# Kernel optimization log

Hardware: AMD Instinct MI355X
Metric: run time of the kernel (lower is better)

## Reference

```python
import jax, jax.numpy as jnp
import numpy as np

N = 100000   # nodes
E = 1200000  # edges
D = 64       # feature dim (in_channels == out_channels)


def gcn_layer(x, W, src, dst):
    # GCNConv(normalize=False, bias=False, aggr='add'):
    # linear transform then scatter-add of source messages into targets.
    h = x @ W                                            # [N, D]
    msg = h[src]                                         # [E, D] gather
    return jax.ops.segment_sum(msg, dst, num_segments=x.shape[0])  # [N, D]


def setup_inputs() -> dict:
    key = jax.random.key(0)
    ks = jax.random.split(key, 5)
    x = jax.random.normal(ks[0], (N, D), dtype=jnp.float32)
    edge_index = jax.random.randint(ks[1], (2, E), 0, N, dtype=jnp.int64)
    scale = 1.0 / np.sqrt(D).astype(np.float32)
    W0 = jax.random.normal(ks[2], (D, D), dtype=jnp.float32) * scale
    W1 = jax.random.normal(ks[3], (D, D), dtype=jnp.float32) * scale
    W2 = jax.random.normal(ks[4], (D, D), dtype=jnp.float32) * scale
    return {"x": x, "edge_index": edge_index, "W0": W0, "W1": W1, "W2": W2}


def reference(x, edge_index, W0, W1, W2):
    src = edge_index[0]  # messages flow source -> target (PyG default)
    dst = edge_index[1]
    # num_hop = 3 stacked convs; dropout p=0 and use_bn=False are no-ops.
    for W in (W0, W1, W2):
        x = gcn_layer(x, W, src, dst)
    return x
```

## Files before the change

kernel.cpp:

```cpp
#include <hip/hip_runtime.h>


#define GCN_D 64
#define SEGSHIFT 8
#define SEGROWS 256
#define MAXSEG 512
#define A_EPB 4096
#define HISTB 512

typedef unsigned short ushort;

__device__ __forceinline__ float bf2f(ushort u) {
    union { unsigned u; float f; } c; c.u = ((unsigned)u) << 16; return c.f;
}
__device__ __forceinline__ float bflo(unsigned u) {
    union { unsigned u; float f; } c; c.u = u << 16; return c.f;
}
__device__ __forceinline__ float bfhi(unsigned u) {
    union { unsigned u; float f; } c; c.u = u & 0xFFFF0000u; return c.f;
}
__device__ __forceinline__ ushort f2bf(float f) {
    union { float f; unsigned u; } c; c.f = f;
    const unsigned r = 0x7FFFu + ((c.u >> 16) & 1u);
    return (ushort)((c.u + r) >> 16);
}
__device__ __forceinline__ unsigned pack2(float a, float b) {
    return (unsigned)f2bf(a) | ((unsigned)f2bf(b) << 16);
}

__global__ __launch_bounds__(256) void k_wchain(const float* __restrict__ W0,
                                                const float* __restrict__ W1,
                                                const float* __restrict__ W2,
                                                float* __restrict__ Wc,
                                                int* __restrict__ ghist,
                                                int* __restrict__ csr0) {
    __shared__ float A[4096], B[4096], T[4096];
    const int t = threadIdx.x;
    for (int i = t; i < MAXSEG; i += 256) { ghist[i] = 0; csr0[i] = 0; }
    for (int i = t; i < 1024; i += 256) {
        ((float4*)A)[i] = ((const float4*)W0)[i];
        ((float4*)B)[i] = ((const float4*)W1)[i];
    }
    __syncthreads();
#pragma unroll
    for (int g = 0; g < 4; ++g) {
        const int idx = t + 256 * g;
        const int r = idx >> 4, c4 = idx & 15;
        float4 acc = make_float4(0.f, 0.f, 0.f, 0.f);
#pragma unroll
        for (int k = 0; k < 64; ++k) {
            const float a = A[r * 64 + k];
            const float4 b = ((float4*)B)[k * 16 + c4];
            acc.x = fmaf(a, b.x, acc.x); acc.y = fmaf(a, b.y, acc.y);
            acc.z = fmaf(a, b.z, acc.z); acc.w = fmaf(a, b.w, acc.w);
        }
        ((float4*)T)[idx] = acc;
    }
    __syncthreads();
    for (int i = t; i < 1024; i += 256) ((float4*)B)[i] = ((const float4*)W2)[i];
    __syncthreads();
#pragma unroll
    for (int g = 0; g < 4; ++g) {
        const int idx = t + 256 * g;
        const int r = idx >> 4, c4 = idx & 15;
        float4 acc = make_float4(0.f, 0.f, 0.f, 0.f);
#pragma unroll
        for (int k = 0; k < 64; ++k) {
            const float a = T[r * 64 + k];
            const float4 b = ((float4*)B)[k * 16 + c4];
            acc.x = fmaf(a, b.x, acc.x); acc.y = fmaf(a, b.y, acc.y);
            acc.z = fmaf(a, b.z, acc.z); acc.w = fmaf(a, b.w, acc.w);
        }
        ((float4*)Wc)[idx] = acc;
    }
}

__global__ __launch_bounds__(256, 3) void k_gemmcvt(const float* __restrict__ X,
                                                    const float* __restrict__ Wc,
                                                    ushort* __restrict__ B,
                                                    const int* __restrict__ ei,
                                                    int* __restrict__ ghist,
                                                    int nrows, int E) {
    __shared__ float Wl[4096];
    __shared__ float Xl[64][68];
    __shared__ int h[MAXSEG];
    const int tid = threadIdx.x;
    for (int i = tid; i < 1024; i += 256) ((float4*)Wl)[i] = ((const float4*)Wc)[i];

    const int rowBase = blockIdx.x * 64;
    for (int i = tid; i < 1024; i += 256) {
        const int r = i >> 4, c4 = i & 15;
        const int gr = rowBase + r;
        const float4 v = (gr < nrows) ? ((const float4*)X)[(size_t)gr * 16 + c4]
                                      : make_float4(0.f, 0.f, 0.f, 0.f);
        *(float4*)&Xl[r][c4 * 4] = v;
    }
    __syncthreads();

    const int tr = tid >> 4;
    const int tc = tid & 15;
    float4 a0 = make_float4(0.f, 0.f, 0.f, 0.f);
    float4 a1 = a0, a2 = a0, a3 = a0;
#pragma unroll 8
    for (int k = 0; k < 64; ++k) {
        const float4 w4 = ((const float4*)Wl)[k * 16 + tc];
        const float x0 = Xl[tr][k];
        const float x1 = Xl[tr + 16][k];
        const float x2 = Xl[tr + 32][k];
        const float x3 = Xl[tr + 48][k];
        a0.x = fmaf(x0, w4.x, a0.x); a0.y = fmaf(x0, w4.y, a0.y);
        a0.z = fmaf(x0, w4.z, a0.z); a0.w = fmaf(x0, w4.w, a0.w);
        a1.x = fmaf(x1, w4.x, a1.x); a1.y = fmaf(x1, w4.y, a1.y);
        a1.z = fmaf(x1, w4.z, a1.z); a1.w = fmaf(x1, w4.w, a1.w);
        a2.x = fmaf(x2, w4.x, a2.x); a2.y = fmaf(x2, w4.y, a2.y);
        a2.z = fmaf(x2, w4.z, a2.z); a2.w = fmaf(x2, w4.w, a2.w);
        a3.x = fmaf(x3, w4.x, a3.x); a3.y = fmaf(x3, w4.y, a3.y);
        a3.z = fmaf(x3, w4.z, a3.z); a3.w = fmaf(x3, w4.w, a3.w);
    }
    {
        const int r0 = rowBase + tr;
        ushort4 o;
        if (r0 < nrows) {
            o.x = f2bf(a0.x); o.y = f2bf(a0.y); o.z = f2bf(a0.z); o.w = f2bf(a0.w);
            ((ushort4*)B)[(size_t)r0 * 16 + tc] = o;
        }
        if (r0 + 16 < nrows) {
            o.x = f2bf(a1.x); o.y = f2bf(a1.y); o.z = f2bf(a1.z); o.w = f2bf(a1.w);
            ((ushort4*)B)[(size_t)(r0 + 16) * 16 + tc] = o;
        }
        if (r0 + 32 < nrows) {
            o.x = f2bf(a2.x); o.y = f2bf(a2.y); o.z = f2bf(a2.z); o.w = f2bf(a2.w);
            ((ushort4*)B)[(size_t)(r0 + 32) * 16 + tc] = o;
        }
        if (r0 + 48 < nrows) {
            o.x = f2bf(a3.x); o.y = f2bf(a3.y); o.z = f2bf(a3.z); o.w = f2bf(a3.w);
            ((ushort4*)B)[(size_t)(r0 + 48) * 16 + tc] = o;
        }
    }

    if (blockIdx.x < HISTB) {
        for (int i = tid; i < MAXSEG; i += 256) h[i] = 0;
        __syncthreads();
        for (int e = blockIdx.x * 256 + tid; e < E; e += HISTB * 256)
            atomicAdd(&h[ei[E + e] >> SEGSHIFT], 1);
        __syncthreads();
        for (int i = tid; i < MAXSEG; i += 256) {
            const int c = h[i];
            if (c) atomicAdd(&ghist[i], c);
        }
    }
}

__global__ __launch_bounds__(512) void k_apart(const int* __restrict__ ei,
                                               const int* __restrict__ ghist,
                                               int* __restrict__ csr0,
                                               unsigned* __restrict__ ebuf, int E) {
    __shared__ int hist[MAXSEG], lofs[MAXSEG], cur[MAXSEG], gbase[MAXSEG], goffx[MAXSEG];
    __shared__ unsigned stg[A_EPB];
    __shared__ ushort stg2[A_EPB];
    const int t = threadIdx.x;
    const int base = blockIdx.x * A_EPB;
    const int cnt = min(A_EPB, E - base);

    const int gv = ghist[t];
    goffx[t] = gv; __syncthreads();
    for (int off = 1; off < MAXSEG; off <<= 1) {
        const int y = (t >= off) ? goffx[t - off] : 0;
        __syncthreads();
        goffx[t] += y;
        __syncthreads();
    }
    const int gexcl = goffx[t] - gv;
    goffx[t] = gexcl;
    hist[t] = 0;
    __syncthreads();

    unsigned my[8]; int mb[8];
#pragma unroll
    for (int j = 0; j < 8; ++j) {
        const int i = t + j * 512;
        if (i < cnt) {
            const int e = base + i;
            const unsigned s = (unsigned)ei[e];
            const unsigned d = (unsigned)ei[E + e];
            my[j] = (s << 8) | (d & (SEGROWS - 1));
            mb[j] = (int)(d >> SEGSHIFT);
            atomicAdd(&hist[mb[j]], 1);
        } else mb[j] = -1;
    }
    __syncthreads();

    {
        const int v = hist[t];
        lofs[t] = v; __syncthreads();
        for (int off = 1; off < MAXSEG; off <<= 1) {
            const int y = (t >= off) ? lofs[t - off] : 0;
            __syncthreads();
            lofs[t] += y;
            __syncthreads();
        }
        const int excl = lofs[t] - v;
        __syncthreads();
        lofs[t] = excl; cur[t] = excl;
    }
    __syncthreads();

#pragma unroll
    for (int j = 0; j < 8; ++j) {
        if (mb[j] >= 0) {
            const int p = atomicAdd(&cur[mb[j]], 1);
            stg[p] = my[j];
            stg2[p] = (ushort)mb[j];
        }
    }
    __syncthreads();

    {
        const int c = hist[t];
        const int p = c ? atomicAdd(&csr0[t], c) : 0;
        gbase[t] = goffx[t] + p;
    }
    __syncthreads();

    for (int i = t; i < cnt; i += 512) {
        const int b = (int)stg2[i];
        ebuf[(size_t)gbase[b] + (unsigned)(i - lofs[b])] = stg[i];
    }
}

__global__ __launch_bounds__(SEGROWS) void k_bplace(const unsigned* __restrict__ ebuf,
                                                    const int* __restrict__ ghist,
                                                    int* __restrict__ rp,
                                                    int* __restrict__ cs, int N, int E) {
    __shared__ int h[SEGROWS], ofs[SEGROWS], gpart[SEGROWS];
    __shared__ int gx[MAXSEG];
    const int s = blockIdx.x;
    const int t = threadIdx.x;

    const int a0 = ghist[2 * t];
    const int a1 = ghist[2 * t + 1];
    const int ps = a0 + a1;
    gpart[t] = ps; __syncthreads();
    for (int off = 1; off < SEGROWS; off <<= 1) {
        const int y = (t >= off) ? gpart[t - off] : 0;
        __syncthreads();
        gpart[t] += y;
        __syncthreads();
    }
    const int ex = gpart[t] - ps;
    gx[2 * t] = ex;
    gx[2 * t + 1] = ex + a0;
    if (s == 0 && t == 0) rp[N] = E;
    __syncthreads();

    const int e0 = gx[s];
    const int e1 = e0 + ghist[s];

    h[t] = 0; __syncthreads();
    for (int e = e0 + t; e < e1; e += SEGROWS)
        atomicAdd(&h[ebuf[e] & (SEGROWS - 1)], 1);
    __syncthreads();

    const int v = h[t];
    ofs[t] = v; __syncthreads();
    for (int off = 1; off < SEGROWS; off <<= 1) {
        const int y = (t >= off) ? ofs[t - off] : 0;
        __syncthreads();
        ofs[t] += y;
        __syncthreads();
    }
    const int excl = ofs[t] - v;
    const int r = s * SEGROWS + t;
    if (r < N) rp[r] = e0 + excl;
    __syncthreads();
    ofs[t] = excl;
    __syncthreads();

    for (int e = e0 + t; e < e1; e += SEGROWS) {
        const unsigned pr = ebuf[e];
        const int lr = (int)(pr & (SEGROWS - 1));
        const int p = atomicAdd(&ofs[lr], 1);
        cs[e0 + p] = (int)(pr >> 8);
    }
}

__global__ __launch_bounds__(256) void k_aggc2(const ushort* __restrict__ B,
                                               const int* __restrict__ rp,
                                               const int* __restrict__ cs,
                                               ushort* __restrict__ out, int N) {
    const int t = threadIdx.x;
    const int gw = (blockIdx.x * 256 + t) >> 6;
    const int lane = t & 63;
    const int f8 = lane & 7;
    const int r = gw * 8 + (lane >> 3);
    if (r >= N) return;

    const int e0 = rp[r];
    const int e1 = rp[r + 1];
    const uint4* Bv = (const uint4*)B;

    float acc[8] = {0.f, 0.f, 0.f, 0.f, 0.f, 0.f, 0.f, 0.f};
    int e = e0;
    for (; e + 7 < e1; e += 8) {
        uint4 u[8];
#pragma unroll
        for (int j = 0; j < 8; ++j) u[j] = Bv[(size_t)cs[e + j] * 8 + f8];
#pragma unroll
        for (int j = 0; j < 8; ++j) {
            acc[0] += bflo(u[j].x); acc[1] += bfhi(u[j].x);
            acc[2] += bflo(u[j].y); acc[3] += bfhi(u[j].y);
            acc[4] += bflo(u[j].z); acc[5] += bfhi(u[j].z);
            acc[6] += bflo(u[j].w); acc[7] += bfhi(u[j].w);
        }
    }
    for (; e < e1; ++e) {
        const uint4 u = Bv[(size_t)cs[e] * 8 + f8];
        acc[0] += bflo(u.x); acc[1] += bfhi(u.x);
        acc[2] += bflo(u.y); acc[3] += bfhi(u.y);
        acc[4] += bflo(u.z); acc[5] += bfhi(u.z);
        acc[6] += bflo(u.w); acc[7] += bfhi(u.w);
    }
    uint4 o;
    o.x = pack2(acc[0], acc[1]); o.y = pack2(acc[2], acc[3]);
    o.z = pack2(acc[4], acc[5]); o.w = pack2(acc[6], acc[7]);
    ((uint4*)out)[(size_t)r * 8 + f8] = o;
}

__global__ __launch_bounds__(256) void k_aggc(const ushort* __restrict__ B,
                                              const int* __restrict__ rp,
                                              const int* __restrict__ cs,
                                              ushort* __restrict__ out, int N) {
    const int t = threadIdx.x;
    const int gw = (blockIdx.x * 256 + t) >> 6;
    const int lane = t & 63;
    const int f4 = lane & 15;
    const int r = gw * 4 + (lane >> 4);
    if (r >= N) return;

    const int e0 = rp[r];
    const int e1 = rp[r + 1];
    const ushort4* Bv = (const ushort4*)B;

    float4 acc = make_float4(0.f, 0.f, 0.f, 0.f);
    int e = e0;
    for (; e + 7 < e1; e += 8) {
        ushort4 u[8];
#pragma unroll
        for (int j = 0; j < 8; ++j) u[j] = Bv[(size_t)cs[e + j] * 16 + f4];
#pragma unroll
        for (int j = 0; j < 8; ++j) {
            acc.x += bf2f(u[j].x); acc.y += bf2f(u[j].y);
            acc.z += bf2f(u[j].z); acc.w += bf2f(u[j].w);
        }
    }
    for (; e + 3 < e1; e += 4) {
        ushort4 u[4];
#pragma unroll
        for (int j = 0; j < 4; ++j) u[j] = Bv[(size_t)cs[e + j] * 16 + f4];
#pragma unroll
        for (int j = 0; j < 4; ++j) {
            acc.x += bf2f(u[j].x); acc.y += bf2f(u[j].y);
            acc.z += bf2f(u[j].z); acc.w += bf2f(u[j].w);
        }
    }
    for (; e < e1; ++e) {
        const ushort4 u = Bv[(size_t)cs[e] * 16 + f4];
        acc.x += bf2f(u.x); acc.y += bf2f(u.y);
        acc.z += bf2f(u.z); acc.w += bf2f(u.w);
    }
    ushort4 o;
    o.x = f2bf(acc.x); o.y = f2bf(acc.y); o.z = f2bf(acc.z); o.w = f2bf(acc.w);
    ((ushort4*)out)[(size_t)r * 16 + f4] = o;
}

__global__ __launch_bounds__(256) void k_aggw(const ushort* __restrict__ B,
                                              const int* __restrict__ rp,
                                              const int* __restrict__ cs,
                                              float* __restrict__ out, int N) {
    const int t = threadIdx.x;
    const int gw = (blockIdx.x * 256 + t) >> 6;
    const int lane = t & 63;
    const int f4 = lane & 15;
    const int r = gw * 4 + (lane >> 4);
    if (r >= N) return;

    const int e0 = rp[r];
    const int e1 = rp[r + 1];
    const ushort4* Bv = (const ushort4*)B;

    float4 acc = make_float4(0.f, 0.f, 0.f, 0.f);
    int e = e0;
    for (; e + 7 < e1; e += 8) {
        ushort4 u[8];
#pragma unroll
        for (int j = 0; j < 8; ++j) u[j] = Bv[(size_t)cs[e + j] * 16 + f4];
#pragma unroll
        for (int j = 0; j < 8; ++j) {
            acc.x += bf2f(u[j].x); acc.y += bf2f(u[j].y);
            acc.z += bf2f(u[j].z); acc.w += bf2f(u[j].w);
        }
    }
    for (; e + 3 < e1; e += 4) {
        ushort4 u[4];
#pragma unroll
        for (int j = 0; j < 4; ++j) u[j] = Bv[(size_t)cs[e + j] * 16 + f4];
#pragma unroll
        for (int j = 0; j < 4; ++j) {
            acc.x += bf2f(u[j].x); acc.y += bf2f(u[j].y);
            acc.z += bf2f(u[j].z); acc.w += bf2f(u[j].w);
        }
    }
    for (; e < e1; ++e) {
        const ushort4 u = Bv[(size_t)cs[e] * 16 + f4];
        acc.x += bf2f(u.x); acc.y += bf2f(u.y);
        acc.z += bf2f(u.z); acc.w += bf2f(u.w);
    }
    ((float4*)out)[(size_t)r * 16 + f4] = acc;
}

__global__ __launch_bounds__(256) void gcn_gemm64(const float* __restrict__ X,
                                                  const float* __restrict__ W,
                                                  float* __restrict__ H,
                                                  int nrows) {
    __shared__ float Wl[64 * 64];
    __shared__ float Xl[16][65];
    const int tid = threadIdx.x;
    for (int i = tid; i < 1024; i += 256) ((float4*)Wl)[i] = ((const float4*)W)[i];
    const int rowBase = blockIdx.x * 16;
    const int lr = tid >> 4;
    const int lc = tid & 15;
    const int grow = rowBase + lr;
    if (grow < nrows) {
        float4 xv = ((const float4*)X)[(long long)grow * 16 + lc];
        Xl[lr][lc * 4 + 0] = xv.x; Xl[lr][lc * 4 + 1] = xv.y;
        Xl[lr][lc * 4 + 2] = xv.z; Xl[lr][lc * 4 + 3] = xv.w;
    }
    __syncthreads();
    float4 acc = make_float4(0.f, 0.f, 0.f, 0.f);
#pragma unroll
    for (int k = 0; k < 64; ++k) {
        const float xv = Xl[lr][k];
        const float4 w4 = ((float4*)Wl)[k * 16 + lc];
        acc.x = fmaf(xv, w4.x, acc.x); acc.y = fmaf(xv, w4.y, acc.y);
        acc.z = fmaf(xv, w4.z, acc.z); acc.w = fmaf(xv, w4.w, acc.w);
    }
    if (grow < nrows) ((float4*)H)[(long long)grow * 16 + lc] = acc;
}

__global__ __launch_bounds__(256) void gcn_scatter(const float* __restrict__ H,
                                                   const int* __restrict__ ei,
                                                   float* __restrict__ out,
                                                   int nedges) {
    const long long t = (long long)blockIdx.x * 256 + threadIdx.x;
    const int e = (int)(t >> 4);
    if (e >= nedges) return;
    const int lc = (int)(t & 15);
    const int s = ei[e];
    const int d = ei[nedges + e];
    const float4 v = ((const float4*)H)[(long long)s * 16 + lc];
    float* o = out + (long long)d * GCN_D + lc * 4;
    atomicAdd(o + 0, v.x);
    atomicAdd(o + 1, v.y);
    atomicAdd(o + 2, v.z);
    atomicAdd(o + 3, v.w);
}

extern "C" void kernel_launch(void* const* d_in, const int* in_sizes, int n_in,
                              void* d_out, int out_size, void* d_ws, size_t ws_size,
                              hipStream_t stream) {
    const float* x  = (const float*)d_in[0];
    const int*   ei = (const int*)d_in[1];
    const float* W0 = (const float*)d_in[2];
    const float* W1 = (const float*)d_in[3];
    const float* W2 = (const float*)d_in[4];
    float* out = (float*)d_out;

    const int N_ = in_sizes[0] / GCN_D;
    const int E_ = in_sizes[1] / 2;
    const int NSEG = (N_ + SEGROWS - 1) >> SEGSHIFT;

    uintptr_t base = (uintptr_t)d_ws;
    ushort* B0 = (ushort*)base;
    const size_t bfBytes  = (size_t)N_ * GCN_D * 2;
    const size_t regBytes = bfBytes > (size_t)E_ * 4 ? bfBytes : (size_t)E_ * 4;
    ushort*   B1   = (ushort*)(base + bfBytes);
    unsigned* ebuf = (unsigned*)B1;
    int* rp    = (int*)(base + bfBytes + regBytes);
    int* ghist = rp + (N_ + 2);
    int* csr0  = ghist + MAXSEG;
    float* Wc  = (float*)(csr0 + MAXSEG);
    int* cs    = (int*)(Wc + 4096);
    const size_t needed = ((uintptr_t)(cs + E_) - base);

    const int gemmBlocks = (N_ + 63) / 64;
    const int gcBlocks = gemmBlocks > HISTB ? gemmBlocks : HISTB;

    if (NSEG <= MAXSEG && N_ < (1 << 24) && ws_size >= needed) {
        k_wchain<<<1, 256, 0, stream>>>(W0, W1, W2, Wc, ghist, csr0);
        k_gemmcvt<<<gcBlocks, 256, 0, stream>>>(x, Wc, B0, ei, ghist, N_, E_);
        k_apart<<<(E_ + A_EPB - 1) / A_EPB, 512, 0, stream>>>(ei, ghist, csr0, ebuf, E_);
        k_bplace<<<NSEG, SEGROWS, 0, stream>>>(ebuf, ghist, rp, cs, N_, E_);

        const int aggBlocks  = (N_ + 15) / 16;
        const int aggBlocks2 = (N_ + 31) / 32;
        k_aggc2<<<aggBlocks2, 256, 0, stream>>>(B0, rp, cs, B1, N_);
        k_aggc <<<aggBlocks,  256, 0, stream>>>(B1, rp, cs, B0, N_);
        k_aggw <<<aggBlocks,  256, 0, stream>>>(B0, rp, cs, out, N_);
    } else {
        float* h = (float*)d_ws;
        const int scatBlocks = (int)(((long long)E_ * 16 + 255) / 256);
        const int gb16 = (N_ + 15) / 16;
        const float* curAct = x;
        for (int l = 0; l < 3; ++l) {
            const float* Wl = (l == 0) ? W0 : (l == 1) ? W1 : W2;
            gcn_gemm64<<<gb16, 256, 0, stream>>>(curAct, Wl, h, N_);
            hipMemsetAsync(out, 0, (size_t)N_ * GCN_D * sizeof(float), stream);
            gcn_scatter<<<scatBlocks, 256, 0, stream>>>(h, ei, out, E_);
            curAct = out;
        }
    }
}
```

Before: 163.3 us.

## Replace global histogram atomics with per-block partial histograms and padded counters

The edge-destination histogram is now computed by 64 blocks that each write a private 512-bin partial histogram instead of atomically adding into one global histogram. Consumers (k_apart, k_bplace) sum the 64 partials themselves. The per-segment cursor counters in csr0 are spaced 16 ints apart to avoid atomic contention on shared cache lines. The intent is to remove global atomic contention, at the cost of fewer histogram blocks (each covering more edges) and redundant partial-sum reads in every downstream block.

```diff
diff --git a/kernel.cpp b/kernel.cpp
--- a/kernel.cpp
+++ b/kernel.cpp
@@ -6,7 +6,8 @@
 #define SEGROWS 256
 #define MAXSEG 512
 #define A_EPB 4096
-#define HISTB 512
+#define NHB 64
+#define CP 16
 
 typedef unsigned short ushort;
 
@@ -32,11 +33,10 @@
                                                 const float* __restrict__ W1,
                                                 const float* __restrict__ W2,
                                                 float* __restrict__ Wc,
-                                                int* __restrict__ ghist,
                                                 int* __restrict__ csr0) {
     __shared__ float A[4096], B[4096], T[4096];
     const int t = threadIdx.x;
-    for (int i = t; i < MAXSEG; i += 256) { ghist[i] = 0; csr0[i] = 0; }
+    for (int i = t; i < MAXSEG * CP; i += 256) csr0[i] = 0;
     for (int i = t; i < 1024; i += 256) {
         ((float4*)A)[i] = ((const float4*)W0)[i];
         ((float4*)B)[i] = ((const float4*)W1)[i];
@@ -79,7 +79,7 @@
                                                     const float* __restrict__ Wc,
                                                     ushort* __restrict__ B,
                                                     const int* __restrict__ ei,
-                                                    int* __restrict__ ghist,
+                                                    int* __restrict__ hs,
                                                     int nrows, int E) {
     __shared__ float Wl[4096];
     __shared__ float Xl[64][68];
@@ -138,21 +138,19 @@
         }
     }
 
-    if (blockIdx.x < HISTB) {
+    if (blockIdx.x < NHB) {
         for (int i = tid; i < MAXSEG; i += 256) h[i] = 0;
         __syncthreads();
-        for (int e = blockIdx.x * 256 + tid; e < E; e += HISTB * 256)
+        for (int e = blockIdx.x * 256 + tid; e < E; e += NHB * 256)
             atomicAdd(&h[ei[E + e] >> SEGSHIFT], 1);
         __syncthreads();
-        for (int i = tid; i < MAXSEG; i += 256) {
-            const int c = h[i];
-            if (c) atomicAdd(&ghist[i], c);
-        }
+        for (int i = tid; i < MAXSEG; i += 256)
+            hs[blockIdx.x * MAXSEG + i] = h[i];
     }
 }
 
 __global__ __launch_bounds__(512) void k_apart(const int* __restrict__ ei,
-                                               const int* __restrict__ ghist,
+                                               const int* __restrict__ hs,
                                                int* __restrict__ csr0,
                                                unsigned* __restrict__ ebuf, int E) {
     __shared__ int hist[MAXSEG], lofs[MAXSEG], cur[MAXSEG], gbase[MAXSEG], goffx[MAXSEG];
@@ -162,7 +160,8 @@
     const int base = blockIdx.x * A_EPB;
     const int cnt = min(A_EPB, E - base);
 
-    const int gv = ghist[t];
+    int gv = 0;
+    for (int b = 0; b < NHB; ++b) gv += hs[b * MAXSEG + t];
     goffx[t] = gv; __syncthreads();
     for (int off = 1; off < MAXSEG; off <<= 1) {
         const int y = (t >= off) ? goffx[t - off] : 0;
@@ -217,7 +216,7 @@
 
     {
         const int c = hist[t];
-        const int p = c ? atomicAdd(&csr0[t], c) : 0;
+        const int p = c ? atomicAdd(&csr0[t * CP], c) : 0;
         gbase[t] = goffx[t] + p;
     }
     __syncthreads();
@@ -229,16 +228,20 @@
 }
 
 __global__ __launch_bounds__(SEGROWS) void k_bplace(const unsigned* __restrict__ ebuf,
-                                                    const int* __restrict__ ghist,
+                                                    const int* __restrict__ hs,
                                                     int* __restrict__ rp,
                                                     int* __restrict__ cs, int N, int E) {
     __shared__ int h[SEGROWS], ofs[SEGROWS], gpart[SEGROWS];
-    __shared__ int gx[MAXSEG];
+    __shared__ int gx[MAXSEG], gcnt[MAXSEG];
     const int s = blockIdx.x;
     const int t = threadIdx.x;
 
-    const int a0 = ghist[2 * t];
-    const int a1 = ghist[2 * t + 1];
+    int a0 = 0, a1 = 0;
+    for (int b = 0; b < NHB; ++b) {
+        a0 += hs[b * MAXSEG + 2 * t];
+        a1 += hs[b * MAXSEG + 2 * t + 1];
+    }
+    gcnt[2 * t] = a0; gcnt[2 * t + 1] = a1;
     const int ps = a0 + a1;
     gpart[t] = ps; __syncthreads();
     for (int off = 1; off < SEGROWS; off <<= 1) {
@@ -254,7 +257,7 @@
     __syncthreads();
 
     const int e0 = gx[s];
-    const int e1 = e0 + ghist[s];
+    const int e1 = e0 + gcnt[s];
 
     h[t] = 0; __syncthreads();
     for (int e = e0 + t; e < e1; e += SEGROWS)
@@ -486,20 +489,20 @@
     ushort*   B1   = (ushort*)(base + bfBytes);
     unsigned* ebuf = (unsigned*)B1;
     int* rp    = (int*)(base + bfBytes + regBytes);
-    int* ghist = rp + (N_ + 2);
-    int* csr0  = ghist + MAXSEG;
-    float* Wc  = (float*)(csr0 + MAXSEG);
+    int* hs    = rp + (N_ + 2);
+    int* csr0  = hs + NHB * MAXSEG;
+    float* Wc  = (float*)(csr0 + MAXSEG * CP);
     int* cs    = (int*)(Wc + 4096);
     const size_t needed = ((uintptr_t)(cs + E_) - base);
 
     const int gemmBlocks = (N_ + 63) / 64;
-    const int gcBlocks = gemmBlocks > HISTB ? gemmBlocks : HISTB;
+    const int gcBlocks = gemmBlocks > NHB ? gemmBlocks : NHB;
 
     if (NSEG <= MAXSEG && N_ < (1 << 24) && ws_size >= needed) {
-        k_wchain<<<1, 256, 0, stream>>>(W0, W1, W2, Wc, ghist, csr0);
-        k_gemmcvt<<<gcBlocks, 256, 0, stream>>>(x, Wc, B0, ei, ghist, N_, E_);
-        k_apart<<<(E_ + A_EPB - 1) / A_EPB, 512, 0, stream>>>(ei, ghist, csr0, ebuf, E_);
-        k_bplace<<<NSEG, SEGROWS, 0, stream>>>(ebuf, ghist, rp, cs, N_, E_);
+        k_wchain<<<1, 256, 0, stream>>>(W0, W1, W2, Wc, csr0);
+        k_gemmcvt<<<gcBlocks, 256, 0, stream>>>(x, Wc, B0, ei, hs, N_, E_);
+        k_apart<<<(E_ + A_EPB - 1) / A_EPB, 512, 0, stream>>>(ei, hs, csr0, ebuf, E_);
+        k_bplace<<<NSEG, SEGROWS, 0, stream>>>(ebuf, hs, rp, cs, N_, E_);
 
         const int aggBlocks  = (N_ + 15) / 16;
         const int aggBlocks2 = (N_ + 31) / 32;
```

New measurement: 167.8 us. +2.7%, slower.
